# Kernel optimization log

Measured on AMD Instinct MI355X. Metric: run time of the kernel, lower is better.

## Reference

```python
import jax, jax.numpy as jnp
import numpy as np

N_NODES = 100000
N_EDGES = 1200000
N_GRAPHS = 128
IN_C, HID_C, OUT_C = 64, 128, 16


def setup_inputs() -> dict:
    key = jax.random.key(0)
    ks = jax.random.split(key, 6)
    x = jax.random.normal(ks[0], (N_NODES, IN_C), dtype=jnp.float32)
    edge_index = jax.random.randint(ks[1], (2, N_EDGES), 0, N_NODES, dtype=jnp.int64)
    batch = jnp.sort(jax.random.randint(ks[2], (N_NODES,), 0, N_GRAPHS, dtype=jnp.int64))
    W1 = jax.random.normal(ks[3], (IN_C, HID_C), dtype=jnp.float32) * (1.0 / np.sqrt(IN_C))
    b1 = jnp.zeros((HID_C,), jnp.float32)
    W2 = jax.random.normal(ks[4], (HID_C, OUT_C), dtype=jnp.float32) * (1.0 / np.sqrt(HID_C))
    b2 = jnp.zeros((OUT_C,), jnp.float32)
    return {"x": x, "edge_index": edge_index, "batch": batch,
            "W1": W1, "b1": b1, "W2": W2, "b2": b2}


def gcn_conv(x, src, dst, W, b, n):
    """PyG GCNConv: add self-loops, symmetric deg^{-1/2} normalization, scatter-add."""
    h = x @ W                                   # [n, out] dense transform first
    loop = jnp.arange(n, dtype=src.dtype)
    s = jnp.concatenate([src, loop])            # edges + self-loops
    d = jnp.concatenate([dst, loop])
    deg = jax.ops.segment_sum(jnp.ones(d.shape[0], h.dtype), d, num_segments=n)
    dinv = jnp.where(deg > 0, jax.lax.rsqrt(deg), jnp.zeros((), h.dtype))
    norm = dinv[s] * dinv[d]                    # [E + n]
    msg = h[s] * norm[:, None]                  # gather + scale
    return jax.ops.segment_sum(msg, d, num_segments=n) + b  # scatter-add


def reference(x, edge_index, batch, W1, b1, W2, b2):
    n = x.shape[0]
    src, dst = edge_index[0], edge_index[1]
    h = jax.nn.relu(gcn_conv(x, src, dst, W1, b1, n))
    h = gcn_conv(h, src, dst, W2, b2, n)
    # global_mean_pool over batch ids
    sums = jax.ops.segment_sum(h, batch, num_segments=N_GRAPHS)
    cnts = jax.ops.segment_sum(jnp.ones((n,), h.dtype), batch, num_segments=N_GRAPHS)
    pooled = sums / jnp.maximum(cnts, 1.0)[:, None]   # [N_GRAPHS, OUT_C]
    return jax.nn.log_softmax(pooled, axis=1)
```

## Files before the change

### kernel.cpp

```cpp
#include <hip/hip_runtime.h>
#include <hip/hip_bf16.h>


#define THREADS 256
#define NPB 256
#define BSTRIDE 4096
#define CH 4096
#define NBMAX 512
#define NGRAPH 128

typedef __attribute__((ext_vector_type(8))) short bf16x8;
typedef __attribute__((ext_vector_type(4))) float f32x4;

__device__ __forceinline__ float bfu_lo(unsigned int u) {
    union { unsigned int i; float f; } v; v.i = u << 16; return v.f;
}
__device__ __forceinline__ float bfu_hi(unsigned int u) {
    union { unsigned int i; float f; } v; v.i = u & 0xffff0000u; return v.f;
}
__device__ __forceinline__ unsigned short f2bf(float f) {
    union { float f; unsigned int i; } v; v.f = f;
    unsigned int r = v.i + 0x7fff + ((v.i >> 16) & 1);
    return (unsigned short)(r >> 16);
}
__device__ __forceinline__ unsigned int packbf(float lo, float hi) {
    return (unsigned int)f2bf(lo) | ((unsigned int)f2bf(hi) << 16);
}
__device__ __forceinline__ void unpack8(uint4 u, float* f) {
    f[0] = bfu_lo(u.x); f[1] = bfu_hi(u.x);
    f[2] = bfu_lo(u.y); f[3] = bfu_hi(u.y);
    f[4] = bfu_lo(u.z); f[5] = bfu_hi(u.z);
    f[6] = bfu_lo(u.w); f[7] = bfu_hi(u.w);
}

__global__ __launch_bounds__(THREADS) void k_partition(const int* __restrict__ src,
                                                       const int* __restrict__ dst,
                                                       int* __restrict__ bucketCursor,
                                                       unsigned int* __restrict__ ebuf,
                                                       int E, int NB) {
    __shared__ int h[NBMAX];
    __shared__ int base[NBMAX];
    __shared__ int cnt[NBMAX];
    __shared__ int dL[CH];
    for (int b = threadIdx.x; b < NBMAX; b += THREADS) { h[b] = 0; cnt[b] = 0; }
    __syncthreads();
    int b0 = blockIdx.x * CH;
    for (int k = 0; k < CH; k += THREADS) {
        int e = b0 + k + threadIdx.x;
        if (e < E) {
            int d = dst[e];
            dL[k + threadIdx.x] = d;
            atomicAdd(&h[d >> 8], 1);
        }
    }
    __syncthreads();
    for (int b = threadIdx.x; b < NB; b += THREADS)
        if (h[b]) base[b] = b * BSTRIDE + atomicAdd(&bucketCursor[b], h[b]);
    __syncthreads();
    for (int k = 0; k < CH; k += THREADS) {
        int e = b0 + k + threadIdx.x;
        if (e < E) {
            int s = src[e];
            int d = dL[k + threadIdx.x];
            int b = d >> 8;
            int i = base[b] + atomicAdd(&cnt[b], 1);
            ebuf[i] = ((unsigned int)(d & (NPB - 1)) << 17) | (unsigned int)s;
        }
    }
}

__global__ __launch_bounds__(THREADS) void k_bucket_csr(const unsigned int* __restrict__ ebuf,
                                                        const int* __restrict__ bucketCursor,
                                                        const float* __restrict__ x,
                                                        int* __restrict__ offs,
                                                        int* __restrict__ deg,
                                                        int* __restrict__ srcs,
                                                        float* __restrict__ dinv,
                                                        uint4* __restrict__ xnb,
                                                        int n) {
    __shared__ unsigned int eL[BSTRIDE];
    __shared__ int c[NPB];
    __shared__ int cur[NPB];
    __shared__ float dloc[NPB];
    __shared__ int sh[THREADS];
    const int tid = threadIdx.x;
    const int b = blockIdx.x;
    const int nbase = b * NPB;
    const int w0 = b * BSTRIDE;
    const int cnt_b = bucketCursor[b];
    c[tid] = 0;
    __syncthreads();
    for (int i = tid; i < cnt_b; i += THREADS) {
        unsigned int e = ebuf[w0 + i];
        eL[i] = e;
        atomicAdd(&c[e >> 17], 1);
    }
    __syncthreads();
    int c0 = c[tid];
    sh[tid] = c0;
    __syncthreads();
    for (int step = 1; step < THREADS; step <<= 1) {
        int t = (tid >= step) ? sh[tid - step] : 0;
        __syncthreads();
        sh[tid] += t;
        __syncthreads();
    }
    int excl = sh[tid] - c0;
    int node = nbase + tid;
    float dv = rsqrtf((float)(c0 + 1));
    dloc[tid] = dv;
    if (node < n) {
        offs[node] = w0 + excl;
        deg[node] = c0;
        dinv[node] = dv;
    }
    cur[tid] = excl;
    __syncthreads();
    for (int i = tid; i < cnt_b; i += THREADS) {
        unsigned int e = eL[i];
        int pos = w0 + atomicAdd(&cur[e >> 17], 1);
        srcs[pos] = (int)(e & 0x1FFFFu);
    }
    const float4* X4 = (const float4*)x;
    for (int i = tid; i < NPB * 8; i += THREADS) {
        int ln = i >> 3;
        int node2 = nbase + ln;
        if (node2 >= n) break;
        int q = i & 7;
        float dd = dloc[ln];
        float4 a = X4[(size_t)node2 * 16 + q * 2];
        float4 bb = X4[(size_t)node2 * 16 + q * 2 + 1];
        uint4 o;
        o.x = packbf(a.x * dd, a.y * dd);
        o.y = packbf(a.z * dd, a.w * dd);
        o.z = packbf(bb.x * dd, bb.y * dd);
        o.w = packbf(bb.z * dd, bb.w * dd);
        xnb[(size_t)node2 * 8 + q] = o;
    }
}

__global__ __launch_bounds__(THREADS) void k_gather1(const int* __restrict__ offs,
                                                     const int* __restrict__ deg,
                                                     const int* __restrict__ srcs,
                                                     const float* __restrict__ dinv,
                                                     const uint4* __restrict__ xnb,
                                                     uint4* __restrict__ aggb, int n) {
    int idx = blockIdx.x * THREADS + threadIdx.x;
    int node = idx >> 3;
    if (node >= n) return;
    int q = idx & 7;
    float acc[8];
    unpack8(xnb[(size_t)node * 8 + q], acc);
    int e0 = offs[node], e1 = e0 + deg[node];
    for (int e = e0; e < e1; ++e) {
        int s = srcs[e];
        float t[8];
        unpack8(xnb[(size_t)s * 8 + q], t);
#pragma unroll
        for (int j = 0; j < 8; ++j) acc[j] += t[j];
    }
    float dd = dinv[node];
    uint4 o;
    o.x = packbf(acc[0] * dd, acc[1] * dd);
    o.y = packbf(acc[2] * dd, acc[3] * dd);
    o.z = packbf(acc[4] * dd, acc[5] * dd);
    o.w = packbf(acc[6] * dd, acc[7] * dd);
    aggb[(size_t)node * 8 + q] = o;
}

__global__ __launch_bounds__(THREADS) void k_gemm12m(const unsigned short* __restrict__ aggb,
                                                     const float* __restrict__ W1,
                                                     const float* __restrict__ b1,
                                                     const float* __restrict__ W2,
                                                     const float* __restrict__ dinv,
                                                     unsigned short* __restrict__ ts,
                                                     int n, int ntiles) {
    __shared__ unsigned short h1L[4][16][136];
    const int wave = threadIdx.x >> 6;
    const int lane = threadIdx.x & 63;
    const int col = lane & 15;
    const int ko = lane >> 4;

    bf16x8 bfr1[2][8];
#pragma unroll
    for (int ks = 0; ks < 2; ++ks)
#pragma unroll
        for (int nt = 0; nt < 8; ++nt) {
            bf16x8 b;
#pragma unroll
            for (int j = 0; j < 8; ++j)
                b[j] = (short)f2bf(W1[(ks * 32 + ko * 8 + j) * 128 + nt * 16 + col]);
            bfr1[ks][nt] = b;
        }
    float bias[8];
#pragma unroll
    for (int nt = 0; nt < 8; ++nt) bias[nt] = b1[nt * 16 + col];
    bf16x8 bfr2[4];
#pragma unroll
    for (int ks = 0; ks < 4; ++ks) {
        bf16x8 b;
#pragma unroll
        for (int j = 0; j < 8; ++j)
            b[j] = (short)f2bf(W2[(ks * 32 + ko * 8 + j) * 16 + col]);
        bfr2[ks] = b;
    }

    const int tile0 = (blockIdx.x * 4 + wave) * 4;
    for (int t = 0; t < 4; ++t) {
        int tile = tile0 + t;
        if (tile >= ntiles) return;
        int r0 = tile * 16;
        int rowA = r0 + col;
        if (rowA >= n) rowA = n - 1;
        const bf16x8* Ap = (const bf16x8*)(aggb + (size_t)rowA * 64 + ko * 8);
        bf16x8 a0 = Ap[0];
        bf16x8 a1 = Ap[4];
        f32x4 acc[8];
#pragma unroll
        for (int nt = 0; nt < 8; ++nt) acc[nt] = (f32x4){0.f, 0.f, 0.f, 0.f};
#pragma unroll
        for (int nt = 0; nt < 8; ++nt) {
            acc[nt] = __builtin_amdgcn_mfma_f32_16x16x32_bf16(a0, bfr1[0][nt], acc[nt], 0, 0, 0);
            acc[nt] = __builtin_amdgcn_mfma_f32_16x16x32_bf16(a1, bfr1[1][nt], acc[nt], 0, 0, 0);
        }
#pragma unroll
        for (int nt = 0; nt < 8; ++nt)
#pragma unroll
            for (int r = 0; r < 4; ++r)
                h1L[wave][ko * 4 + r][nt * 16 + col] = f2bf(fmaxf(acc[nt][r] + bias[nt], 0.f));
        f32x4 acc2 = (f32x4){0.f, 0.f, 0.f, 0.f};
#pragma unroll
        for (int ks = 0; ks < 4; ++ks) {
            bf16x8 a2 = *(const bf16x8*)&h1L[wave][col][ks * 32 + ko * 8];
            acc2 = __builtin_amdgcn_mfma_f32_16x16x32_bf16(a2, bfr2[ks], acc2, 0, 0, 0);
        }
#pragma unroll
        for (int r = 0; r < 4; ++r) {
            int row = r0 + ko * 4 + r;
            if (row < n) {
                float dd = dinv[row];
                ts[(size_t)row * 16 + col] = f2bf(acc2[r] * dd);
            }
        }
    }
}

__global__ __launch_bounds__(THREADS) void k_gatherpool(const int* __restrict__ offs,
                                                        const int* __restrict__ deg,
                                                        const int* __restrict__ srcs,
                                                        const float* __restrict__ dinv,
                                                        const uint4* __restrict__ ts,
                                                        const int* __restrict__ batch,
                                                        float* __restrict__ sums, int n) {
    __shared__ float gsum[NGRAPH * 16];
    const int tid = threadIdx.x;
    for (int i = tid; i < NGRAPH * 16; i += THREADS) gsum[i] = 0.f;
    __syncthreads();
    int idx = blockIdx.x * THREADS + tid;
    int node = idx >> 1;
    if (node < n) {
        int q = idx & 1;
        float acc[8];
        unpack8(ts[(size_t)node * 2 + q], acc);
        int e0 = offs[node], e1 = e0 + deg[node];
        for (int e = e0; e < e1; ++e) {
            int s = srcs[e];
            float t[8];
            unpack8(ts[(size_t)s * 2 + q], t);
#pragma unroll
            for (int j = 0; j < 8; ++j) acc[j] += t[j];
        }
        float dd = dinv[node];
        int g = batch[node];
        float* row = &gsum[g * 16 + q * 8];
#pragma unroll
        for (int j = 0; j < 8; ++j) atomicAdd(&row[j], acc[j] * dd);
    }
    __syncthreads();
    for (int i = tid; i < NGRAPH * 16; i += THREADS) {
        float v = gsum[i];
        if (v != 0.f) atomicAdd(&sums[i], v);
    }
}

__global__ __launch_bounds__(NGRAPH) void k_final(const float* __restrict__ sums,
                                                  const int* __restrict__ batch,
                                                  const float* __restrict__ b2,
                                                  float* __restrict__ out, int n) {
    int g = threadIdx.x;
    int lo = 0, hi = n;
    while (lo < hi) { int mid = (lo + hi) >> 1; if (batch[mid] < g) lo = mid + 1; else hi = mid; }
    int s0 = lo;
    hi = n;
    while (lo < hi) { int mid = (lo + hi) >> 1; if (batch[mid] < g + 1) lo = mid + 1; else hi = mid; }
    int s1 = lo;
    float cnt = fmaxf((float)(s1 - s0), 1.0f);
    float v[16];
    float mx = -1e30f;
#pragma unroll
    for (int c = 0; c < 16; ++c) {
        v[c] = sums[g * 16 + c] / cnt + b2[c];
        mx = fmaxf(mx, v[c]);
    }
    float se = 0.f;
#pragma unroll
    for (int c = 0; c < 16; ++c) se += expf(v[c] - mx);
    float lse = logf(se) + mx;
#pragma unroll
    for (int c = 0; c < 16; ++c) out[g * 16 + c] = v[c] - lse;
}

extern "C" void kernel_launch(void* const* d_in, const int* in_sizes, int n_in,
                              void* d_out, int out_size, void* d_ws, size_t ws_size,
                              hipStream_t stream) {
    const float* x    = (const float*)d_in[0];
    const int* edges  = (const int*)d_in[1];
    const int* batch  = (const int*)d_in[2];
    const float* W1   = (const float*)d_in[3];
    const float* b1   = (const float*)d_in[4];
    const float* W2   = (const float*)d_in[5];
    const float* b2   = (const float*)d_in[6];
    float* out        = (float*)d_out;

    const int n = in_sizes[2];
    const int E = in_sizes[1] / 2;
    const int* src = edges;
    const int* dst = edges + E;
    const int NB = (n + NPB - 1) / NPB;
    const int npart = (E + CH - 1) / CH;
    const int ntiles = (n + 15) / 16;

    char* ws = (char*)d_ws;
    size_t off = 0;
    auto carve = [&](size_t bytes) { char* p = ws + off; off = (off + bytes + 255) & ~(size_t)255; return p; };
    int*   bucketCursor = (int*)carve(NBMAX * 4);
    float* sums    = (float*)carve(NGRAPH * 16 * 4);
    int*   offs    = (int*)carve((size_t)n * 4);
    int*   deg     = (int*)carve((size_t)n * 4);
    int*   srcs    = (int*)carve((size_t)NB * BSTRIDE * 4);
    float* dinv    = (float*)carve((size_t)n * 4);
    uint4* xnb     = (uint4*)carve((size_t)n * 64 * 2);
    char*  aggreg  = (char*)carve((size_t)n * 64 * 2);
    char*  big     = (char*)carve((size_t)NB * BSTRIDE * 4 > (size_t)n * 128 * 2
                                  ? (size_t)NB * BSTRIDE * 4 : (size_t)n * 128 * 2);
    unsigned int* ebuf = (unsigned int*)big;
    unsigned short* ts = (unsigned short*)big;
    unsigned short* aggb = (unsigned short*)aggreg;

    auto blks = [](long long work) { return (int)((work + THREADS - 1) / THREADS); };

    hipMemsetAsync(bucketCursor, 0, NBMAX * 4 + NGRAPH * 16 * 4, stream);
    k_partition  <<<npart, THREADS, 0, stream>>>(src, dst, bucketCursor, ebuf, E, NB);
    k_bucket_csr <<<NB, THREADS, 0, stream>>>(ebuf, bucketCursor, x, offs, deg, srcs, dinv, xnb, n);

    k_gather1 <<<blks((long long)n * 8), THREADS, 0, stream>>>(offs, deg, srcs, dinv, xnb, (uint4*)aggb, n);
    k_gemm12m <<<(ntiles + 15) / 16, THREADS, 0, stream>>>(aggb, W1, b1, W2, dinv, ts, n, ntiles);

    k_gatherpool <<<blks((long long)n * 2), THREADS, 0, stream>>>(offs, deg, srcs, dinv,
                                                                  (const uint4*)ts, batch, sums, n);
    k_final <<<1, NGRAPH, 0, stream>>>(sums, batch, b2, out, n);
}
```

Before: 129.0 us.

## Degree-sort nodes per bucket, unroll gathers, fuse final softmax into pooling

Builds a per-bucket permutation of nodes sorted by in-degree so gather wavefronts process nodes of similar degree, reducing lane divergence in the edge loops. Unrolls both gather loops by two to expose more independent loads. Removes the separate final kernel by having the last block of the pooling kernel (detected via an atomic counter) compute the mean and log-softmax. Adds an indirection through perm and scattered output writes, plus a threadfence/atomic tail.

```diff
diff --git a/kernel.cpp b/kernel.cpp
--- a/kernel.cpp
+++ b/kernel.cpp
@@ -77,18 +77,22 @@
                                                         int* __restrict__ srcs,
                                                         float* __restrict__ dinv,
                                                         uint4* __restrict__ xnb,
+                                                        int* __restrict__ perm,
                                                         int n) {
     __shared__ unsigned int eL[BSTRIDE];
     __shared__ int c[NPB];
     __shared__ int cur[NPB];
     __shared__ float dloc[NPB];
     __shared__ int sh[THREADS];
+    __shared__ int dbin[64];
+    __shared__ int dbase[64];
     const int tid = threadIdx.x;
     const int b = blockIdx.x;
     const int nbase = b * NPB;
     const int w0 = b * BSTRIDE;
     const int cnt_b = bucketCursor[b];
     c[tid] = 0;
+    if (tid < 64) dbin[tid] = 0;
     __syncthreads();
     for (int i = tid; i < cnt_b; i += THREADS) {
         unsigned int e = ebuf[w0 + i];
@@ -98,6 +102,12 @@
     __syncthreads();
     int c0 = c[tid];
     sh[tid] = c0;
+    int node = nbase + tid;
+    int rank = 0, db = 0;
+    if (node < n) {
+        db = min(c0, 63);
+        rank = atomicAdd(&dbin[db], 1);
+    }
     __syncthreads();
     for (int step = 1; step < THREADS; step <<= 1) {
         int t = (tid >= step) ? sh[tid - step] : 0;
@@ -105,8 +115,11 @@
         sh[tid] += t;
         __syncthreads();
     }
+    if (tid == 0) {
+        int run = 0;
+        for (int i = 0; i < 64; ++i) { dbase[i] = run; run += dbin[i]; }
+    }
     int excl = sh[tid] - c0;
-    int node = nbase + tid;
     float dv = rsqrtf((float)(c0 + 1));
     dloc[tid] = dv;
     if (node < n) {
@@ -116,6 +129,7 @@
     }
     cur[tid] = excl;
     __syncthreads();
+    if (node < n) perm[nbase + dbase[db] + rank] = node;
     for (int i = tid; i < cnt_b; i += THREADS) {
         unsigned int e = eL[i];
         int pos = w0 + atomicAdd(&cur[e >> 17], 1);
@@ -144,15 +158,26 @@
                                                      const int* __restrict__ srcs,
                                                      const float* __restrict__ dinv,
                                                      const uint4* __restrict__ xnb,
+                                                     const int* __restrict__ perm,
                                                      uint4* __restrict__ aggb, int n) {
     int idx = blockIdx.x * THREADS + threadIdx.x;
-    int node = idx >> 3;
-    if (node >= n) return;
+    int nid = idx >> 3;
+    if (nid >= n) return;
+    int node = perm[nid];
     int q = idx & 7;
     float acc[8];
     unpack8(xnb[(size_t)node * 8 + q], acc);
     int e0 = offs[node], e1 = e0 + deg[node];
-    for (int e = e0; e < e1; ++e) {
+    int e = e0;
+    for (; e + 1 < e1; e += 2) {
+        int s0 = srcs[e], s1 = srcs[e + 1];
+        float t0[8], t1[8];
+        unpack8(xnb[(size_t)s0 * 8 + q], t0);
+        unpack8(xnb[(size_t)s1 * 8 + q], t1);
+#pragma unroll
+        for (int j = 0; j < 8; ++j) acc[j] += t0[j] + t1[j];
+    }
+    if (e < e1) {
         int s = srcs[e];
         float t[8];
         unpack8(xnb[(size_t)s * 8 + q], t);
@@ -251,19 +276,34 @@
                                                         const float* __restrict__ dinv,
                                                         const uint4* __restrict__ ts,
                                                         const int* __restrict__ batch,
-                                                        float* __restrict__ sums, int n) {
+                                                        const int* __restrict__ perm,
+                                                        float* __restrict__ sums,
+                                                        int* __restrict__ donecnt,
+                                                        const float* __restrict__ b2,
+                                                        float* __restrict__ out, int n) {
     __shared__ float gsum[NGRAPH * 16];
+    __shared__ int lastFlag;
     const int tid = threadIdx.x;
     for (int i = tid; i < NGRAPH * 16; i += THREADS) gsum[i] = 0.f;
     __syncthreads();
     int idx = blockIdx.x * THREADS + tid;
-    int node = idx >> 1;
-    if (node < n) {
+    int nid = idx >> 1;
+    if (nid < n) {
+        int node = perm[nid];
         int q = idx & 1;
         float acc[8];
         unpack8(ts[(size_t)node * 2 + q], acc);
         int e0 = offs[node], e1 = e0 + deg[node];
-        for (int e = e0; e < e1; ++e) {
+        int e = e0;
+        for (; e + 1 < e1; e += 2) {
+            int s0 = srcs[e], s1 = srcs[e + 1];
+            float t0[8], t1[8];
+            unpack8(ts[(size_t)s0 * 2 + q], t0);
+            unpack8(ts[(size_t)s1 * 2 + q], t1);
+#pragma unroll
+            for (int j = 0; j < 8; ++j) acc[j] += t0[j] + t1[j];
+        }
+        if (e < e1) {
             int s = srcs[e];
             float t[8];
             unpack8(ts[(size_t)s * 2 + q], t);
@@ -281,33 +321,32 @@
         float v = gsum[i];
         if (v != 0.f) atomicAdd(&sums[i], v);
     }
-}
-
-__global__ __launch_bounds__(NGRAPH) void k_final(const float* __restrict__ sums,
-                                                  const int* __restrict__ batch,
-                                                  const float* __restrict__ b2,
-                                                  float* __restrict__ out, int n) {
-    int g = threadIdx.x;
-    int lo = 0, hi = n;
-    while (lo < hi) { int mid = (lo + hi) >> 1; if (batch[mid] < g) lo = mid + 1; else hi = mid; }
-    int s0 = lo;
-    hi = n;
-    while (lo < hi) { int mid = (lo + hi) >> 1; if (batch[mid] < g + 1) lo = mid + 1; else hi = mid; }
-    int s1 = lo;
-    float cnt = fmaxf((float)(s1 - s0), 1.0f);
-    float v[16];
-    float mx = -1e30f;
-#pragma unroll
-    for (int c = 0; c < 16; ++c) {
-        v[c] = sums[g * 16 + c] / cnt + b2[c];
-        mx = fmaxf(mx, v[c]);
-    }
-    float se = 0.f;
-#pragma unroll
-    for (int c = 0; c < 16; ++c) se += expf(v[c] - mx);
-    float lse = logf(se) + mx;
-#pragma unroll
-    for (int c = 0; c < 16; ++c) out[g * 16 + c] = v[c] - lse;
+    __threadfence();
+    if (tid == 0) lastFlag = (atomicAdd(donecnt, 1) == (int)gridDim.x - 1);
+    __syncthreads();
+    if (lastFlag && tid < NGRAPH) {
+        __threadfence();
+        int g = tid;
+        int lo = 0, hi = n;
+        while (lo < hi) { int mid = (lo + hi) >> 1; if (batch[mid] < g) lo = mid + 1; else hi = mid; }
+        int s0 = lo;
+        hi = n;
+        while (lo < hi) { int mid = (lo + hi) >> 1; if (batch[mid] < g + 1) lo = mid + 1; else hi = mid; }
+        float cnt = fmaxf((float)(lo - s0), 1.0f);
+        float v[16];
+        float mx = -1e30f;
+#pragma unroll
+        for (int c = 0; c < 16; ++c) {
+            v[c] = atomicAdd(&sums[g * 16 + c], 0.0f) / cnt + b2[c];
+            mx = fmaxf(mx, v[c]);
+        }
+        float se = 0.f;
+#pragma unroll
+        for (int c = 0; c < 16; ++c) se += expf(v[c] - mx);
+        float lse = logf(se) + mx;
+#pragma unroll
+        for (int c = 0; c < 16; ++c) out[g * 16 + c] = v[c] - lse;
+    }
 }
 
 extern "C" void kernel_launch(void* const* d_in, const int* in_sizes, int n_in,
@@ -335,8 +374,10 @@
     auto carve = [&](size_t bytes) { char* p = ws + off; off = (off + bytes + 255) & ~(size_t)255; return p; };
     int*   bucketCursor = (int*)carve(NBMAX * 4);
     float* sums    = (float*)carve(NGRAPH * 16 * 4);
+    int*   donecnt = (int*)carve(256);
     int*   offs    = (int*)carve((size_t)n * 4);
     int*   deg     = (int*)carve((size_t)n * 4);
+    int*   perm    = (int*)carve((size_t)n * 4);
     int*   srcs    = (int*)carve((size_t)NB * BSTRIDE * 4);
     float* dinv    = (float*)carve((size_t)n * 4);
     uint4* xnb     = (uint4*)carve((size_t)n * 64 * 2);
@@ -349,14 +390,14 @@
 
     auto blks = [](long long work) { return (int)((work + THREADS - 1) / THREADS); };
 
-    hipMemsetAsync(bucketCursor, 0, NBMAX * 4 + NGRAPH * 16 * 4, stream);
+    hipMemsetAsync(bucketCursor, 0, NBMAX * 4 + NGRAPH * 16 * 4 + 256, stream);
     k_partition  <<<npart, THREADS, 0, stream>>>(src, dst, bucketCursor, ebuf, E, NB);
-    k_bucket_csr <<<NB, THREADS, 0, stream>>>(ebuf, bucketCursor, x, offs, deg, srcs, dinv, xnb, n);
-
-    k_gather1 <<<blks((long long)n * 8), THREADS, 0, stream>>>(offs, deg, srcs, dinv, xnb, (uint4*)aggb, n);
+    k_bucket_csr <<<NB, THREADS, 0, stream>>>(ebuf, bucketCursor, x, offs, deg, srcs, dinv, xnb, perm, n);
+
+    k_gather1 <<<blks((long long)n * 8), THREADS, 0, stream>>>(offs, deg, srcs, dinv, xnb, perm, (uint4*)aggb, n);
     k_gemm12m <<<(ntiles + 15) / 16, THREADS, 0, stream>>>(aggb, W1, b1, W2, dinv, ts, n, ntiles);
 
     k_gatherpool <<<blks((long long)n * 2), THREADS, 0, stream>>>(offs, deg, srcs, dinv,
-                                                                  (const uint4*)ts, batch, sums, n);
-    k_final <<<1, NGRAPH, 0, stream>>>(sums, batch, b2, out, n);
-}
+                                                                  (const uint4*)ts, batch, perm,
+                                                                  sums, donecnt, b2, out, n);
+}
```

Result: slower. 170.0 us (+31.8%).
